# Kernel optimization log

Measured on AMD Instinct MI355X. Metric: run time of the kernel, lower is better.

## Reference

```python
import jax, jax.numpy as jnp
import numpy as np

EMBED = 1024
HEADS = 16
DK = EMBED // HEADS
DFF = 4 * EMBED
EPS = 1e-5


def layer_norm(x, g, b):
    mu = jnp.mean(x, axis=-1, keepdims=True)
    var = jnp.var(x, axis=-1, keepdims=True)
    return (x - mu) * jax.lax.rsqrt(var + EPS) * g + b


def setup_inputs() -> dict:
    key = jax.random.key(0)
    ks = jax.random.split(key, 12)
    s = lambda d: 1.0 / np.sqrt(d)
    return {
        "x": jax.random.normal(ks[0], (4, 1024, EMBED), dtype=jnp.float32),
        "norm_g": jnp.ones((EMBED,), jnp.float32),
        "norm_b": jnp.zeros((EMBED,), jnp.float32),
        "w_qkv": jax.random.normal(ks[1], (EMBED, 3 * EMBED), jnp.float32) * s(EMBED),
        "b_qkv": jnp.zeros((3 * EMBED,), jnp.float32),
        "w_proj": jax.random.normal(ks[2], (EMBED, EMBED), jnp.float32) * s(EMBED),
        "b_proj": jnp.zeros((EMBED,), jnp.float32),
        "w_fc1": jax.random.normal(ks[3], (EMBED, DFF), jnp.float32) * s(EMBED),
        "b_fc1": jnp.zeros((DFF,), jnp.float32),
        "w_fc2": jax.random.normal(ks[4], (DFF, EMBED), jnp.float32) * s(DFF),
        "b_fc2": jnp.zeros((EMBED,), jnp.float32),
    }


def reference(x, norm_g, norm_b, w_qkv, b_qkv, w_proj, b_proj, w_fc1, b_fc1, w_fc2, b_fc2):
    B, N, C = x.shape
    # --- attention branch (pre-norm, shared norm params) ---
    h = layer_norm(x, norm_g, norm_b)
    qkv = (h @ w_qkv + b_qkv).reshape(B, N, 3, HEADS, DK)
    q, k, v = jnp.moveaxis(qkv, 2, 0)  # each [B, N, H, dk]
    # NOTE: source divides by dk**(-0.5), i.e. multiplies scores by sqrt(dk)
    scores = jnp.einsum('bnhd,bmhd->bhnm', q, k) * (DK ** 0.5)
    attn = jax.nn.softmax(scores, axis=-1)
    ctx = jnp.einsum('bhnm,bmhd->bnhd', attn, v).reshape(B, N, C)
    x = x + (ctx @ w_proj + b_proj)
    # --- MLP branch ---
    h = layer_norm(x, norm_g, norm_b)
    h = jax.nn.gelu(h @ w_fc1 + b_fc1, approximate=False)
    x = x + (h @ w_fc2 + b_fc2)
    return x
```

## Files before the change

kernel.cpp:

```cpp
#include <hip/hip_runtime.h>
#include <hip/hip_bf16.h>

typedef __attribute__((ext_vector_type(8))) short short8;
typedef __attribute__((ext_vector_type(8))) _Float16 half8;
typedef __attribute__((ext_vector_type(4))) float f32x4;

__device__ __forceinline__ unsigned short f2h(float f) {
    _Float16 h = (_Float16)f;
    return *reinterpret_cast<unsigned short*>(&h);
}
__device__ __forceinline__ float h2f(unsigned short u) {
    _Float16 h = *reinterpret_cast<_Float16*>(&u);
    return (float)h;
}

__device__ __forceinline__ void gld_lds16(const unsigned short* g, unsigned short* l) {
    __builtin_amdgcn_global_load_lds(
        (const __attribute__((address_space(1))) unsigned int*)g,
        (__attribute__((address_space(3))) unsigned int*)l, 16, 0, 0);
}

__global__ __launch_bounds__(256)
void transpose_all(const float* __restrict__ W0, const float* __restrict__ W1,
                   const float* __restrict__ W2, const float* __restrict__ W3,
                   unsigned short* __restrict__ o0, unsigned short* __restrict__ o1,
                   unsigned short* __restrict__ o2, unsigned short* __restrict__ o3) {
    __shared__ float tile[32][33];
    const int bid = blockIdx.x;
    const float* W; unsigned short* out; int K, N, loc;
    if (bid < 3072)      { W = W0; out = o0; K = 1024; N = 3072; loc = bid; }
    else if (bid < 4096) { W = W1; out = o1; K = 1024; N = 1024; loc = bid - 3072; }
    else if (bid < 8192) { W = W2; out = o2; K = 1024; N = 4096; loc = bid - 4096; }
    else                 { W = W3; out = o3; K = 4096; N = 1024; loc = bid - 8192; }
    const int nx = N >> 5;
    const int n0 = (loc % nx) << 5, k0 = (loc / nx) << 5;
    const int tid = threadIdx.x;
    const int r = tid >> 3, c4 = (tid & 7) << 2;
    float4 v = *reinterpret_cast<const float4*>(W + (size_t)(k0 + r) * N + n0 + c4);
    tile[r][c4 + 0] = v.x; tile[r][c4 + 1] = v.y;
    tile[r][c4 + 2] = v.z; tile[r][c4 + 3] = v.w;
    __syncthreads();
    const int n = n0 + r;
    ushort4 o;
    o.x = f2h(tile[c4 + 0][r]); o.y = f2h(tile[c4 + 1][r]);
    o.z = f2h(tile[c4 + 2][r]); o.w = f2h(tile[c4 + 3][r]);
    *reinterpret_cast<ushort4*>(out + (size_t)n * K + k0 + c4) = o;
}

template<int IN16>
__global__ __launch_bounds__(256)
void ln_kernel(const void* __restrict__ xin, const float* __restrict__ gw,
               const float* __restrict__ bw, unsigned short* __restrict__ out) {
    const int row = blockIdx.x, tid = threadIdx.x;
    float v0, v1, v2, v3;
    if (IN16) {
        const unsigned short* xr = (const unsigned short*)xin + (size_t)row * 1024;
        ushort4 u = *reinterpret_cast<const ushort4*>(xr + tid * 4);
        v0 = h2f(u.x); v1 = h2f(u.y); v2 = h2f(u.z); v3 = h2f(u.w);
    } else {
        const float* xr = (const float*)xin + (size_t)row * 1024;
        float4 v = *reinterpret_cast<const float4*>(xr + tid * 4);
        v0 = v.x; v1 = v.y; v2 = v.z; v3 = v.w;
    }
    float s = v0 + v1 + v2 + v3;
    float sq = v0 * v0 + v1 * v1 + v2 * v2 + v3 * v3;
    #pragma unroll
    for (int off = 1; off < 64; off <<= 1) {
        s  += __shfl_xor(s, off);
        sq += __shfl_xor(sq, off);
    }
    __shared__ float ps[4], pq[4];
    const int wave = tid >> 6;
    if ((tid & 63) == 0) { ps[wave] = s; pq[wave] = sq; }
    __syncthreads();
    s  = ps[0] + ps[1] + ps[2] + ps[3];
    sq = pq[0] + pq[1] + pq[2] + pq[3];
    const float mu = s * (1.0f / 1024.0f);
    const float var = sq * (1.0f / 1024.0f) - mu * mu;
    const float rs = rsqrtf(var + 1e-5f);
    float4 gv = *reinterpret_cast<const float4*>(gw + tid * 4);
    float4 bv = *reinterpret_cast<const float4*>(bw + tid * 4);
    ushort4 o;
    o.x = f2h((v0 - mu) * rs * gv.x + bv.x);
    o.y = f2h((v1 - mu) * rs * gv.y + bv.y);
    o.z = f2h((v2 - mu) * rs * gv.z + bv.z);
    o.w = f2h((v3 - mu) * rs * gv.w + bv.w);
    *reinterpret_cast<ushort4*>(out + (size_t)row * 1024 + tid * 4) = o;
}

template<int EPI, int NZ>
__global__ __launch_bounds__(512, 4)
void gemm_mid(const unsigned short* __restrict__ A, const unsigned short* __restrict__ Bt,
              const float* __restrict__ bias, void* Cout,
              int M, int N, int K, int lda, int ldb, int ldc) {
    __shared__ unsigned short As[2][128 * 32];
    __shared__ unsigned short Bs[2][256 * 32];
    const int tid = threadIdx.x;
    const int wave = tid >> 6, lane = tid & 63;
    const int nx = N >> 8;
    int bm, bn, z;
    if (NZ == 1) {
        const int nwg = gridDim.x;
        const int swz = (blockIdx.x & 7) * (nwg >> 3) + (blockIdx.x >> 3);
        bm = (swz / nx) << 7; bn = (swz % nx) << 8; z = 0;
    } else {
        int bid = blockIdx.x;
        const int xcd = bid & 7; int rest = bid >> 3;
        bn = (rest % nx) << 8; rest /= nx;
        z = rest % NZ; rest /= NZ;
        bm = (rest * 8 + xcd) << 7;
    }
    const size_t koff = (size_t)z * K;
    const int wm = wave >> 2, wn = wave & 3;
    const int fr = lane & 15, g8 = (lane >> 4) << 3, fq = (lane >> 4) << 2;
    const int jq = g8 >> 3;
    const int sx2 = (fr >> 1) & 3;

    const int srow = lane >> 2;
    const int scol = ((lane & 3) ^ ((lane >> 3) & 3)) << 3;
    const unsigned short* gA  = A + (size_t)(bm + wave * 16 + srow) * lda + scol + koff;
    const unsigned short* gB0 = Bt + (size_t)(bn + wave * 32 + srow) * ldb + scol + koff;
    const unsigned short* gB1 = gB0 + (size_t)16 * ldb;
    const int lbA = wave * 512;
    const int lbB = wave * 1024;

    f32x4 acc[4][4];
    #pragma unroll
    for (int m = 0; m < 4; ++m)
        #pragma unroll
        for (int n_ = 0; n_ < 4; ++n_)
            #pragma unroll
            for (int r_ = 0; r_ < 4; ++r_) acc[m][n_][r_] = 0.0f;

    auto stage = [&](int buf, int k0) {
        gld_lds16(gA + k0, &As[buf][lbA]);
        gld_lds16(gB0 + k0, &Bs[buf][lbB]);
        gld_lds16(gB1 + k0, &Bs[buf][lbB + 512]);
    };
    auto compute = [&](int buf) {
        half8 af[4], bfv[4];
        #pragma unroll
        for (int m = 0; m < 4; ++m)
            af[m] = *reinterpret_cast<const half8*>(
                &As[buf][(wm * 64 + m * 16 + fr) * 32 + ((jq ^ sx2) << 3)]);
        #pragma unroll
        for (int n_ = 0; n_ < 4; ++n_)
            bfv[n_] = *reinterpret_cast<const half8*>(
                &Bs[buf][(wn * 64 + n_ * 16 + fr) * 32 + ((jq ^ sx2) << 3)]);
        #pragma unroll
        for (int m = 0; m < 4; ++m)
            #pragma unroll
            for (int n_ = 0; n_ < 4; ++n_)
                acc[m][n_] = __builtin_amdgcn_mfma_f32_16x16x32_f16(af[m], bfv[n_], acc[m][n_], 0, 0, 0);
    };

    const int nt = K >> 5;
    stage(0, 0);
    __syncthreads();
    int k0 = 32;
    for (int t = 0; t < nt - 2; t += 2) {
        stage(1, k0);
        compute(0);
        __syncthreads();
        stage(0, k0 + 32);
        compute(1);
        __syncthreads();
        k0 += 64;
    }
    stage(1, k0);
    compute(0);
    __syncthreads();
    compute(1);

    if (EPI == 4) {
        unsigned short* P = reinterpret_cast<unsigned short*>(Cout) +
                            (size_t)z * (size_t)M * ldc;
        #pragma unroll
        for (int n_ = 0; n_ < 4; ++n_) {
            const int col = bn + wn * 64 + n_ * 16 + fr;
            #pragma unroll
            for (int m = 0; m < 4; ++m)
                #pragma unroll
                for (int r_ = 0; r_ < 4; ++r_) {
                    const int row = bm + wm * 64 + m * 16 + fq + r_;
                    P[(size_t)row * ldc + col] = f2h(acc[m][n_][r_]);
                }
        }
        return;
    }

    unsigned short* o16 = reinterpret_cast<unsigned short*>(Cout);
    #pragma unroll
    for (int n_ = 0; n_ < 4; ++n_) {
        const int col = bn + wn * 64 + n_ * 16 + fr;
        const float bc = bias[col];
        #pragma unroll
        for (int m = 0; m < 4; ++m) {
            #pragma unroll
            for (int r_ = 0; r_ < 4; ++r_) {
                const int row = bm + wm * 64 + m * 16 + fq + r_;
                const size_t idx = (size_t)row * ldc + col;
                float v = acc[m][n_][r_] + bc;
                if (EPI == 0) {
                    o16[idx] = f2h(v);
                } else {
                    float ge = 0.5f * v * (1.0f + erff(v * 0.70710678118654752f));
                    o16[idx] = f2h(ge);
                }
            }
        }
    }
}

template<int EPI, int BM, int REMAP>
__global__ __launch_bounds__(256)
void gemm_bt(const unsigned short* __restrict__ A, const unsigned short* __restrict__ Bt,
             const float* __restrict__ bias, const float* resid,
             void* Cout, int M, int N, int K, int lda, int ldb, int ldc) {
    constexpr int MF = BM / 32;
    __shared__ unsigned short As[2][BM * 32];
    __shared__ unsigned short Bs[2][128 * 32];
    const int tid = threadIdx.x;
    const int wave = tid >> 6, lane = tid & 63;
    int bm, bn;
    if (REMAP) {
        const int nxr = N >> 7;
        int bid = blockIdx.x;
        const int xcd = bid & 7; int rest = bid >> 3;
        bn = (rest % nxr) << 7; rest /= nxr;
        bm = (rest * 8 + xcd) * BM;
    } else {
        bm = blockIdx.y * BM; bn = blockIdx.x << 7;
    }
    const int wr = (wave >> 1) * (BM / 2), wc = (wave & 1) << 6;
    const int fr = lane & 15, g8 = (lane >> 4) << 3, fq = (lane >> 4) << 2;
    const int jq = g8 >> 3, sx2 = (fr >> 1) & 3;

    const int srowA = (BM == 128) ? ((wave << 5) + (lane >> 2)) : ((wave << 4) + (lane >> 2));
    const int srowB = (wave << 5) + (lane >> 2);
    const int scol = (((lane & 3) ^ ((lane >> 3) & 3))) << 3;
    const unsigned short* gA0 = A + (size_t)(bm + srowA) * lda + scol;
    const unsigned short* gA1 = gA0 + (size_t)16 * lda;
    const unsigned short* gB0 = Bt + (size_t)(bn + srowB) * ldb + scol;
    const unsigned short* gB1 = gB0 + (size_t)16 * ldb;

    f32x4 acc[MF][4];
    #pragma unroll
    for (int m = 0; m < MF; ++m)
        #pragma unroll
        for (int n = 0; n < 4; ++n)
            #pragma unroll
            for (int r = 0; r < 4; ++r) acc[m][n][r] = 0.0f;

    auto stage = [&](int buf, int k0) {
        unsigned short* lA = &As[buf][(BM == 128) ? (wave << 10) : (wave << 9)];
        unsigned short* lB = &Bs[buf][wave << 10];
        gld_lds16(gA0 + k0, lA);
        if constexpr (BM == 128) gld_lds16(gA1 + k0, lA + 512);
        gld_lds16(gB0 + k0, lB);
        gld_lds16(gB1 + k0, lB + 512);
    };
    auto compute = [&](int buf) {
        half8 af[MF], bfv[4];
        #pragma unroll
        for (int m = 0; m < MF; ++m)
            af[m] = *reinterpret_cast<const half8*>(
                &As[buf][(wr + m * 16 + fr) * 32 + ((jq ^ sx2) << 3)]);
        #pragma unroll
        for (int n = 0; n < 4; ++n)
            bfv[n] = *reinterpret_cast<const half8*>(
                &Bs[buf][(wc + n * 16 + fr) * 32 + ((jq ^ sx2) << 3)]);
        #pragma unroll
        for (int m = 0; m < MF; ++m)
            #pragma unroll
            for (int n = 0; n < 4; ++n)
                acc[m][n] = __builtin_amdgcn_mfma_f32_16x16x32_f16(af[m], bfv[n], acc[m][n], 0, 0, 0);
    };

    const int nt = K >> 5;
    stage(0, 0);
    __syncthreads();
    int k0 = 32;
    for (int t = 0; t < nt - 2; t += 2) {
        stage(1, k0);
        compute(0);
        __syncthreads();
        stage(0, k0 + 32);
        compute(1);
        __syncthreads();
        k0 += 64;
    }
    stage(1, k0);
    compute(0);
    __syncthreads();
    compute(1);

    #pragma unroll
    for (int n = 0; n < 4; ++n) {
        const int col = bn + wc + n * 16 + fr;
        const float bc = bias[col];
        #pragma unroll
        for (int m = 0; m < MF; ++m) {
            #pragma unroll
            for (int r = 0; r < 4; ++r) {
                const int row = bm + wr + m * 16 + fq + r;
                const size_t idx = (size_t)row * ldc + col;
                float v = acc[m][n][r] + bc;
                reinterpret_cast<unsigned short*>(Cout)[idx] = f2h(v + resid[idx]);
            }
        }
    }
}

template<int Z>
__global__ __launch_bounds__(256)
void red_h(const unsigned short* __restrict__ p, const unsigned short* __restrict__ x1h,
           const float* __restrict__ bias, float* out) {
    const size_t MN = (size_t)4096 * 1024;
    const size_t i = ((size_t)blockIdx.x * 256 + threadIdx.x) * 4;
    ushort4 xh = *reinterpret_cast<const ushort4*>(x1h + i);
    float4 bb = *reinterpret_cast<const float4*>(bias + (i & 1023));
    float o0 = h2f(xh.x) + bb.x, o1 = h2f(xh.y) + bb.y;
    float o2 = h2f(xh.z) + bb.z, o3 = h2f(xh.w) + bb.w;
    #pragma unroll
    for (int z = 0; z < Z; ++z) {
        ushort4 a = *reinterpret_cast<const ushort4*>(p + (size_t)z * MN + i);
        o0 += h2f(a.x); o1 += h2f(a.y); o2 += h2f(a.z); o3 += h2f(a.w);
    }
    float4 o; o.x = o0; o.y = o1; o.z = o2; o.w = o3;
    *reinterpret_cast<float4*>(out + i) = o;
}

__global__ __launch_bounds__(256)
void kv_conv(const unsigned short* __restrict__ qkv16, unsigned short* __restrict__ K_g,
             unsigned short* __restrict__ Vt_g) {
    __shared__ unsigned short VtT[64][72];
    const int kc = blockIdx.x;
    const int bh = blockIdx.y;
    const int b = bh >> 4, h = bh & 15;
    const int tid = threadIdx.x;
    const int key = tid >> 2, c16 = (tid & 3) << 4;
    const unsigned short* kp = qkv16 + ((size_t)(b * 1024 + kc * 64 + key)) * 3072 + 1024 + h * 64 + c16;
    alignas(16) unsigned short kbuf[16];
    const float KSCALE = 8.0f * 1.44269504088896f;
    #pragma unroll
    for (int j = 0; j < 16; j += 8) {
        short8 k8 = *reinterpret_cast<const short8*>(kp + j);
        short8 v8 = *reinterpret_cast<const short8*>(kp + 1024 + j);
        #pragma unroll
        for (int c = 0; c < 8; ++c) {
            kbuf[j + c] = f2h(KSCALE * h2f((unsigned short)k8[c]));
            VtT[c16 + j + c][key] = (unsigned short)v8[c];
        }
    }
    const size_t kb = ((size_t)bh * 1024 + kc * 64 + key) * 64 + c16;
    *reinterpret_cast<short8*>(K_g + kb)     = *reinterpret_cast<short8*>(&kbuf[0]);
    *reinterpret_cast<short8*>(K_g + kb + 8) = *reinterpret_cast<short8*>(&kbuf[8]);
    __syncthreads();
    const int d = tid >> 2;
    const size_t vb = ((size_t)bh * 64 + d) * 1024 + (size_t)kc * 64 + c16;
    *reinterpret_cast<short8*>(Vt_g + vb)     = *reinterpret_cast<const short8*>(&VtT[d][c16]);
    *reinterpret_cast<short8*>(Vt_g + vb + 8) = *reinterpret_cast<const short8*>(&VtT[d][c16 + 8]);
}

__global__ __launch_bounds__(256)
void attn_kernel(const unsigned short* __restrict__ qkv16,
                 const unsigned short* __restrict__ K_g,
                 const unsigned short* __restrict__ Vt_g,
                 unsigned short* __restrict__ ctx) {
    __shared__ unsigned short Kh[64][72];
    __shared__ unsigned short Vt[64][72];
    __shared__ unsigned short Plds[4][16][72];
    const int bh = blockIdx.x;
    const int qt = blockIdx.y;
    const int b = bh >> 4, h = bh & 15;
    const int tid = threadIdx.x;
    const int wave = tid >> 6, lane = tid & 63;
    const int fr = lane & 15, g8 = (lane >> 4) << 3, fq = (lane >> 4) << 2;

    const int qrow = qt * 64 + wave * 16 + fr;
    const unsigned short* qp = qkv16 + ((size_t)(b * 1024 + qrow)) * 3072 + h * 64;
    half8 qf[2];
    qf[0] = *reinterpret_cast<const half8*>(qp + g8);
    qf[1] = *reinterpret_cast<const half8*>(qp + 32 + g8);

    half8 ones;
    #pragma unroll
    for (int j = 0; j < 8; ++j) ones[j] = (_Float16)1.0f;

    float mrun[4];
    f32x4 cacc[4], csum;
    #pragma unroll
    for (int r = 0; r < 4; ++r) { mrun[r] = -3.0e38f; csum[r] = 0.0f; }
    #pragma unroll
    for (int nd = 0; nd < 4; ++nd)
        #pragma unroll
        for (int r = 0; r < 4; ++r) cacc[nd][r] = 0.0f;

    const int skey = tid >> 2, sc16 = (tid & 3) << 4;
    const unsigned short* kgp = K_g + ((size_t)bh * 1024 + skey) * 64 + sc16;
    const unsigned short* vgp = Vt_g + ((size_t)bh * 64 + skey) * 1024 + sc16;

    short8 ka = *reinterpret_cast<const short8*>(kgp);
    short8 kb = *reinterpret_cast<const short8*>(kgp + 8);
    short8 va = *reinterpret_cast<const short8*>(vgp);
    short8 vb = *reinterpret_cast<const short8*>(vgp + 8);

    for (int kt = 0; kt < 16; ++kt) {
        __syncthreads();
        *reinterpret_cast<short8*>(&Kh[skey][sc16])     = ka;
        *reinterpret_cast<short8*>(&Kh[skey][sc16 + 8]) = kb;
        *reinterpret_cast<short8*>(&Vt[skey][sc16])     = va;
        *reinterpret_cast<short8*>(&Vt[skey][sc16 + 8]) = vb;
        __syncthreads();
        const int ktn = (kt < 15) ? kt + 1 : 15;
        ka = *reinterpret_cast<const short8*>(kgp + (size_t)ktn * 4096);
        kb = *reinterpret_cast<const short8*>(kgp + (size_t)ktn * 4096 + 8);
        va = *reinterpret_cast<const short8*>(vgp + ktn * 64);
        vb = *reinterpret_cast<const short8*>(vgp + ktn * 64 + 8);

        f32x4 S[4];
        #pragma unroll
        for (int n = 0; n < 4; ++n)
            #pragma unroll
            for (int r = 0; r < 4; ++r) S[n][r] = 0.0f;
        #pragma unroll
        for (int s_ = 0; s_ < 2; ++s_)
            #pragma unroll
            for (int n = 0; n < 4; ++n) {
                half8 kh = *reinterpret_cast<const half8*>(&Kh[n * 16 + fr][s_ * 32 + g8]);
                S[n] = __builtin_amdgcn_mfma_f32_16x16x32_f16(qf[s_], kh, S[n], 0, 0, 0);
            }

        float mt[4];
        #pragma unroll
        for (int r = 0; r < 4; ++r)
            mt[r] = fmaxf(fmaxf(S[0][r], S[1][r]), fmaxf(S[2][r], S[3][r]));
        #pragma unroll
        for (int r = 0; r < 4; ++r) {
            mt[r] = fmaxf(mt[r], __shfl_xor(mt[r], 1));
            mt[r] = fmaxf(mt[r], __shfl_xor(mt[r], 2));
            mt[r] = fmaxf(mt[r], __shfl_xor(mt[r], 4));
            mt[r] = fmaxf(mt[r], __shfl_xor(mt[r], 8));
        }
        int grow = 0;
        #pragma unroll
        for (int r = 0; r < 4; ++r) grow |= (mt[r] > mrun[r] + 8.0f) ? 1 : 0;
        if (__any(grow)) {
            #pragma unroll
            for (int r = 0; r < 4; ++r) {
                float mnew = fmaxf(mrun[r], mt[r]);
                float sf = __builtin_amdgcn_exp2f(mrun[r] - mnew);
                mrun[r] = mnew;
                csum[r] *= sf;
                #pragma unroll
                for (int nd = 0; nd < 4; ++nd) cacc[nd][r] *= sf;
            }
        }
        #pragma unroll
        for (int r = 0; r < 4; ++r)
            #pragma unroll
            for (int n = 0; n < 4; ++n)
                Plds[wave][fq + r][n * 16 + fr] =
                    f2h(__builtin_amdgcn_exp2f(S[n][r] - mrun[r]));
        #pragma unroll
        for (int s_ = 0; s_ < 2; ++s_) {
            half8 pa = *reinterpret_cast<const half8*>(&Plds[wave][fr][s_ * 32 + g8]);
            #pragma unroll
            for (int nd = 0; nd < 4; ++nd) {
                half8 vb8 = *reinterpret_cast<const half8*>(&Vt[nd * 16 + fr][s_ * 32 + g8]);
                cacc[nd] = __builtin_amdgcn_mfma_f32_16x16x32_f16(pa, vb8, cacc[nd], 0, 0, 0);
            }
            csum = __builtin_amdgcn_mfma_f32_16x16x32_f16(pa, ones, csum, 0, 0, 0);
        }
    }
    #pragma unroll
    for (int r = 0; r < 4; ++r) {
        const float inv = 1.0f / csum[r];
        const int row = qt * 64 + wave * 16 + fq + r;
        unsigned short* cp = ctx + ((size_t)(b * 1024 + row)) * 1024 + h * 64;
        #pragma unroll
        for (int nd = 0; nd < 4; ++nd)
            cp[nd * 16 + fr] = f2h(cacc[nd][r] * inv);
    }
}

extern "C" void kernel_launch(void* const* d_in, const int* in_sizes, int n_in,
                              void* d_out, int out_size, void* d_ws, size_t ws_size,
                              hipStream_t stream) {
    const float* x      = (const float*)d_in[0];
    const float* norm_g = (const float*)d_in[1];
    const float* norm_b = (const float*)d_in[2];
    const float* w_qkv  = (const float*)d_in[3];
    const float* b_qkv  = (const float*)d_in[4];
    const float* w_proj = (const float*)d_in[5];
    const float* b_proj = (const float*)d_in[6];
    const float* w_fc1  = (const float*)d_in[7];
    const float* b_fc1  = (const float*)d_in[8];
    const float* w_fc2  = (const float*)d_in[9];
    const float* b_fc2  = (const float*)d_in[10];
    float* out = (float*)d_out;
    char* ws = (char*)d_ws;

    size_t off = 0;
    unsigned short* wqkvT  = (unsigned short*)(ws + off); off += (size_t)3072 * 1024 * 2;
    unsigned short* wprojT = (unsigned short*)(ws + off); off += (size_t)1024 * 1024 * 2;
    unsigned short* wfc1T  = (unsigned short*)(ws + off); off += (size_t)4096 * 1024 * 2;
    unsigned short* wfc2T  = (unsigned short*)(ws + off); off += (size_t)1024 * 4096 * 2;
    unsigned short* ctxb   = (unsigned short*)(ws + off); off += (size_t)4096 * 1024 * 2;
    char* G = ws + off;
    unsigned short* h1    = (unsigned short*)G;
    unsigned short* qkv16 = (unsigned short*)(G + (size_t)8388608);
    unsigned short* K_g   = (unsigned short*)G;
    unsigned short* Vt_g  = (unsigned short*)(G + (size_t)33554432);
    unsigned short* fc1o  = (unsigned short*)G;
    unsigned short* h2    = (unsigned short*)(G + (size_t)41943040);
    unsigned short* fc2ph = (unsigned short*)(G + (size_t)33554432);
    unsigned short* x1h   = (unsigned short*)(G + (size_t)67108864);

    transpose_all<<<12288, 256, 0, stream>>>(w_qkv, w_proj, w_fc1, w_fc2,
                                             wqkvT, wprojT, wfc1T, wfc2T);

    ln_kernel<0><<<4096, 256, 0, stream>>>(x, norm_g, norm_b, h1);
    gemm_mid<0, 1><<<384, 512, 0, stream>>>(h1, wqkvT, b_qkv, qkv16,
                                            4096, 3072, 1024, 1024, 1024, 3072);

    kv_conv<<<dim3(16, 64), 256, 0, stream>>>(qkv16, K_g, Vt_g);

    attn_kernel<<<dim3(64, 16), 256, 0, stream>>>(qkv16, K_g, Vt_g, ctxb);

    gemm_bt<5, 64, 1><<<512, 256, 0, stream>>>(ctxb, wprojT, b_proj, x, x1h,
                                               4096, 1024, 1024, 1024, 1024, 1024);

    ln_kernel<1><<<4096, 256, 0, stream>>>(x1h, norm_g, norm_b, h2);
    gemm_mid<2, 1><<<512, 512, 0, stream>>>(h2, wfc1T, b_fc1, fc1o,
                                            4096, 4096, 1024, 1024, 1024, 4096);

    gemm_mid<4, 4><<<512, 512, 0, stream>>>(fc1o, wfc2T, nullptr, fc2ph,
                                            4096, 1024, 1024, 4096, 4096, 1024);
    red_h<4><<<4096, 256, 0, stream>>>(fc2ph, x1h, b_fc2, out);
}
```

Measured before the change: 244.8 us.

## Load K/V MFMA fragments directly from global memory, drop LDS staging and barriers

The attention kernel no longer stages K and V tiles in shared memory with two block barriers per key tile. Each wave now loads its MFMA operand fragments for K and V^T straight from global memory, relying on L1/L2 caching because all four waves read the same data. The change also adds s_setprio around the MFMA blocks and a min-blocks-per-CU hint on launch bounds. It removes synchronisation and LDS traffic, but each tile is now fetched four times through the cache and there is no longer a prefetch of the next tile.

Measured after the change: 311.1 us. 1.27x slower.

```diff
diff --git a/kernel.cpp b/kernel.cpp
--- a/kernel.cpp
+++ b/kernel.cpp
@@ -363,13 +363,11 @@
     *reinterpret_cast<short8*>(Vt_g + vb + 8) = *reinterpret_cast<const short8*>(&VtT[d][c16 + 8]);
 }
 
-__global__ __launch_bounds__(256)
+__global__ __launch_bounds__(256, 4)
 void attn_kernel(const unsigned short* __restrict__ qkv16,
                  const unsigned short* __restrict__ K_g,
                  const unsigned short* __restrict__ Vt_g,
                  unsigned short* __restrict__ ctx) {
-    __shared__ unsigned short Kh[64][72];
-    __shared__ unsigned short Vt[64][72];
     __shared__ unsigned short Plds[4][16][72];
     const int bh = blockIdx.x;
     const int qt = blockIdx.y;
@@ -397,40 +395,38 @@
         #pragma unroll
         for (int r = 0; r < 4; ++r) cacc[nd][r] = 0.0f;
 
-    const int skey = tid >> 2, sc16 = (tid & 3) << 4;
-    const unsigned short* kgp = K_g + ((size_t)bh * 1024 + skey) * 64 + sc16;
-    const unsigned short* vgp = Vt_g + ((size_t)bh * 64 + skey) * 1024 + sc16;
-
-    short8 ka = *reinterpret_cast<const short8*>(kgp);
-    short8 kb = *reinterpret_cast<const short8*>(kgp + 8);
-    short8 va = *reinterpret_cast<const short8*>(vgp);
-    short8 vb = *reinterpret_cast<const short8*>(vgp + 8);
+    const unsigned short* Kfb = K_g + ((size_t)bh * 1024 + fr) * 64 + g8;
+    const unsigned short* Vfb = Vt_g + ((size_t)bh * 64 + fr) * 1024 + g8;
 
     for (int kt = 0; kt < 16; ++kt) {
-        __syncthreads();
-        *reinterpret_cast<short8*>(&Kh[skey][sc16])     = ka;
-        *reinterpret_cast<short8*>(&Kh[skey][sc16 + 8]) = kb;
-        *reinterpret_cast<short8*>(&Vt[skey][sc16])     = va;
-        *reinterpret_cast<short8*>(&Vt[skey][sc16 + 8]) = vb;
-        __syncthreads();
-        const int ktn = (kt < 15) ? kt + 1 : 15;
-        ka = *reinterpret_cast<const short8*>(kgp + (size_t)ktn * 4096);
-        kb = *reinterpret_cast<const short8*>(kgp + (size_t)ktn * 4096 + 8);
-        va = *reinterpret_cast<const short8*>(vgp + ktn * 64);
-        vb = *reinterpret_cast<const short8*>(vgp + ktn * 64 + 8);
+        const unsigned short* Kt = Kfb + (size_t)kt * 4096;
+        half8 kh[2][4];
+        #pragma unroll
+        for (int n = 0; n < 4; ++n) {
+            kh[0][n] = *reinterpret_cast<const half8*>(Kt + n * 1024);
+            kh[1][n] = *reinterpret_cast<const half8*>(Kt + n * 1024 + 32);
+        }
 
         f32x4 S[4];
         #pragma unroll
         for (int n = 0; n < 4; ++n)
             #pragma unroll
             for (int r = 0; r < 4; ++r) S[n][r] = 0.0f;
+        __builtin_amdgcn_s_setprio(1);
         #pragma unroll
         for (int s_ = 0; s_ < 2; ++s_)
             #pragma unroll
-            for (int n = 0; n < 4; ++n) {
-                half8 kh = *reinterpret_cast<const half8*>(&Kh[n * 16 + fr][s_ * 32 + g8]);
-                S[n] = __builtin_amdgcn_mfma_f32_16x16x32_f16(qf[s_], kh, S[n], 0, 0, 0);
-            }
+            for (int n = 0; n < 4; ++n)
+                S[n] = __builtin_amdgcn_mfma_f32_16x16x32_f16(qf[s_], kh[s_][n], S[n], 0, 0, 0);
+        __builtin_amdgcn_s_setprio(0);
+
+        const unsigned short* Vt = Vfb + kt * 64;
+        half8 vv[2][4];
+        #pragma unroll
+        for (int nd = 0; nd < 4; ++nd) {
+            vv[0][nd] = *reinterpret_cast<const half8*>(Vt + (size_t)nd * 16384);
+            vv[1][nd] = *reinterpret_cast<const half8*>(Vt + (size_t)nd * 16384 + 32);
+        }
 
         float mt[4];
         #pragma unroll
@@ -463,16 +459,16 @@
             for (int n = 0; n < 4; ++n)
                 Plds[wave][fq + r][n * 16 + fr] =
                     f2h(__builtin_amdgcn_exp2f(S[n][r] - mrun[r]));
+        __builtin_amdgcn_s_setprio(1);
         #pragma unroll
         for (int s_ = 0; s_ < 2; ++s_) {
             half8 pa = *reinterpret_cast<const half8*>(&Plds[wave][fr][s_ * 32 + g8]);
             #pragma unroll
-            for (int nd = 0; nd < 4; ++nd) {
-                half8 vb8 = *reinterpret_cast<const half8*>(&Vt[nd * 16 + fr][s_ * 32 + g8]);
-                cacc[nd] = __builtin_amdgcn_mfma_f32_16x16x32_f16(pa, vb8, cacc[nd], 0, 0, 0);
-            }
+            for (int nd = 0; nd < 4; ++nd)
+                cacc[nd] = __builtin_amdgcn_mfma_f32_16x16x32_f16(pa, vv[s_][nd], cacc[nd], 0, 0, 0);
             csum = __builtin_amdgcn_mfma_f32_16x16x32_f16(pa, ones, csum, 0, 0, 0);
         }
+        __builtin_amdgcn_s_setprio(0);
     }
     #pragma unroll
     for (int r = 0; r < 4; ++r) {
```
